# Performance work log

Hardware: AMD Instinct MI355X
Metric: run time of the kernel (lower is better)

Reference implementation:

```python
import jax, jax.numpy as jnp
import numpy as np

B, D, H, T = 8192, 256, 512, 4  # batch, latent dim, hidden units, num IAF transforms


def _made_masks():
    deg_in = np.arange(1, D + 1)                      # input degrees 1..D
    deg_h = 1 + (np.arange(H) % (D - 1))              # hidden degrees in [1, D-1]
    m1 = (deg_h[None, :] >= deg_in[:, None]).astype(np.float32)   # [D, H]
    m2 = (deg_h[None, :] >= deg_h[:, None]).astype(np.float32)    # [H, H]
    mo = (deg_in[None, :] > deg_h[:, None]).astype(np.float32)    # [H, D] strict for outputs
    m3 = np.repeat(mo, 2, axis=1)                     # [H, 2D]: params=2 per dim, interleaved
    return jnp.asarray(m1), jnp.asarray(m2), jnp.asarray(m3)

M1, M2, M3 = _made_masks()


def _made(x, w1, b1, w2, b2, w3, b3):
    h = jax.nn.relu(x @ (w1 * M1) + b1)
    h = jax.nn.relu(h @ (w2 * M2) + b2)
    out = (h @ (w3 * M3) + b3).reshape(x.shape[0], D, 2)
    shift, log_var = out[..., 0], out[..., 1]
    # lstm_flag == False branch of Made.call
    return shift, jnp.tanh(log_var)


def setup_inputs() -> dict:
    key = jax.random.key(0)
    ks = jax.random.split(key, 6)
    s1 = 0.05
    return {
        "mean": jax.random.normal(ks[0], (B, D), jnp.float32),
        "log_var": jax.random.normal(ks[1], (B, D), jnp.float32) * 0.5,
        "eps": jax.random.normal(ks[2], (B, D), jnp.float32),
        "W1": jax.random.normal(ks[3], (T, D, H), jnp.float32) * s1,
        "b1": jnp.zeros((T, H), jnp.float32),
        "W2": jax.random.normal(ks[4], (T, H, H), jnp.float32) * s1,
        "b2": jnp.zeros((T, H), jnp.float32),
        "W3": jax.random.normal(ks[5], (T, H, 2 * D), jnp.float32) * s1,
        "b3": jnp.zeros((T, 2 * D), jnp.float32),
    }


def reference(mean, log_var, eps, W1, b1, W2, b2, W3, b3):
    # Base sample from MultivariateNormalDiag(mean, exp(0.5*log_var))
    x = mean + jnp.exp(0.5 * log_var) * eps
    # Chain([IAF_0, Perm, IAF_1, Perm, ..., IAF_{T-1}, Perm]).forward applies the
    # LAST bijector first: Perm, then Invert(MAF)_{T-1}, ..., down to IAF_0.
    # Invert(MAF).forward == MAF.inverse: a single parallel MADE pass.
    for i in reversed(range(T)):
        x = x[..., ::-1]  # Permute(reversed(range(D)))
        shift, log_scale = _made(x, W1[i], b1[i], W2[i], b2[i], W3[i], b3[i])
        x = (x - shift) * jnp.exp(-log_scale)
    return x
```

## Files before the change

kernel.cpp:

```cpp
#include <hip/hip_runtime.h>


typedef _Float16 f16;
typedef __attribute__((ext_vector_type(8))) _Float16 f16x8;
typedef __attribute__((ext_vector_type(4))) float f32x4;

#define NB 8192
#define ND 256
#define NH 512
#define NT 4
#define XSTR 260

#define W1F_OFF 0
#define W2F_OFF (NT*NH*ND)
#define W3F_OFF (W2F_OFF + NT*NH*NH)
#define WS_ELEMS (W3F_OFF + NT*NH*NH)

__device__ __forceinline__ int h_orig(int j) {
  if (j < 3) return j == 0 ? 0 : (j == 1 ? 255 : 510);
  if (j < 6) return j == 3 ? 1 : (j == 4 ? 256 : 511);
  int d = j >> 1;
  return (j & 1) ? (d + 254) : (d - 1);
}
__device__ __forceinline__ int h_deg(int j) {
  return (j < 3) ? 1 : (j < 6) ? 2 : (j >> 1);
}

__global__ void prep_weights(const float* __restrict__ W1,
                             const float* __restrict__ W2,
                             const float* __restrict__ W3,
                             f16* __restrict__ ws)
{
  int idx = blockIdx.x * blockDim.x + threadIdx.x;
  if (idx >= WS_ELEMS) return;
  float v;
  if (idx < W2F_OFF) {
    int t = idx >> 17, r = idx & ((1 << 17) - 1);
    int e = r & 7, lane = (r >> 3) & 63, ks = (r >> 9) & 7, tile = r >> 12;
    int j = tile * 16 + (lane & 15);
    int k = ks * 32 + (lane >> 4) * 8 + e;
    v = (k <= h_deg(j) - 1) ? W1[t * (ND * NH) + k * NH + h_orig(j)] : 0.f;
  } else if (idx < W3F_OFF) {
    int q = idx - W2F_OFF;
    int t = q >> 18, r = q & ((1 << 18) - 1);
    int e = r & 7, lane = (r >> 3) & 63, ks = (r >> 9) & 15, tile = r >> 13;
    int j = tile * 16 + (lane & 15);
    int k = ks * 32 + (lane >> 4) * 8 + e;
    v = (h_deg(k) <= h_deg(j)) ? W2[t * (NH * NH) + h_orig(k) * NH + h_orig(j)] : 0.f;
  } else {
    int q = idx - W3F_OFF;
    int t = q >> 18, r = q & ((1 << 18) - 1);
    int e = r & 7, lane = (r >> 3) & 63, ks = (r >> 9) & 15, tile = r >> 13;
    int n = tile * 16 + (lane & 15);
    int k = ks * 32 + (lane >> 4) * 8 + e;
    v = (h_deg(k) <= (n >> 1)) ? W3[t * (NH * 2 * ND) + h_orig(k) * (2 * ND) + n] : 0.f;
  }
  ws[idx] = (f16)v;
}

#define MFMA16 __builtin_amdgcn_mfma_f32_16x16x32_f16

template<int SSTRB>
__device__ __forceinline__ void gemm_hybrid(const f16* srcA,
                                            const f16* __restrict__ wtS,
                                            const f16* __restrict__ wtB,
                                            int ncS, int ncB,
                                            int lrow, int lk8,
                                            f32x4 &aS0, f32x4 &aS1,
                                            f32x4 &aB0, f32x4 &aB1)
{
  const f32x4 z = {0.f, 0.f, 0.f, 0.f};
  aS0 = z; aS1 = z; aB0 = z; aB1 = z;
  const int r1 = 16 + lrow;
  const int swz0 = (lrow & 7) << 4;
  const int swz1 = (r1 & 7) << 4;

  f16x8 cS0 = *(const f16x8*)(wtS);
  f16x8 cS1 = *(const f16x8*)(wtS + 512);
  f16x8 cB0 = *(const f16x8*)(wtB);
  f16x8 cB1 = *(const f16x8*)(wtB + 512);
  for (int c = 0; ; ++c) {
    f16x8 nS0, nS1, nB0, nB1;
    const bool more = (c + 1 < ncS);
    if (more) {
      const f16* pS = wtS + (c + 1) * 1024;
      const f16* pB = wtB + (c + 1) * 1024;
      nS0 = *(const f16x8*)(pS);
      nS1 = *(const f16x8*)(pS + 512);
      nB0 = *(const f16x8*)(pB);
      nB1 = *(const f16x8*)(pB + 512);
    }
    #pragma unroll
    for (int u = 0; u < 2; ++u) {
      int kb = 128 * c + u * 64 + lk8 * 16;
      f16x8 a0 = *(const f16x8*)((const char*)srcA + ((lrow * SSTRB + kb) ^ swz0));
      f16x8 a1 = *(const f16x8*)((const char*)srcA + ((r1 * SSTRB + kb) ^ swz1));
      f16x8 bS = u ? cS1 : cS0;
      f16x8 bB = u ? cB1 : cB0;
      aS0 = MFMA16(a0, bS, aS0, 0, 0, 0);
      aS1 = MFMA16(a1, bS, aS1, 0, 0, 0);
      aB0 = MFMA16(a0, bB, aB0, 0, 0, 0);
      aB1 = MFMA16(a1, bB, aB1, 0, 0, 0);
    }
    if (!more) break;
    cS0 = nS0; cS1 = nS1; cB0 = nB0; cB1 = nB1;
  }

  if (ncS < ncB) {
    f16x8 dB0 = *(const f16x8*)(wtB + ncS * 1024);
    f16x8 dB1 = *(const f16x8*)(wtB + ncS * 1024 + 512);
    for (int c = ncS; ; ++c) {
      f16x8 nB0, nB1;
      const bool more = (c + 1 < ncB);
      if (more) {
        const f16* pB = wtB + (c + 1) * 1024;
        nB0 = *(const f16x8*)(pB);
        nB1 = *(const f16x8*)(pB + 512);
      }
      #pragma unroll
      for (int u = 0; u < 2; ++u) {
        int kb = 128 * c + u * 64 + lk8 * 16;
        f16x8 a0 = *(const f16x8*)((const char*)srcA + ((lrow * SSTRB + kb) ^ swz0));
        f16x8 a1 = *(const f16x8*)((const char*)srcA + ((r1 * SSTRB + kb) ^ swz1));
        f16x8 bB = u ? dB1 : dB0;
        aB0 = MFMA16(a0, bB, aB0, 0, 0, 0);
        aB1 = MFMA16(a1, bB, aB1, 0, 0, 0);
      }
      if (!more) break;
      dB0 = nB0; dB1 = nB1;
    }
  }
}

__device__ __forceinline__ void epi_relu_tile(f32x4 a0, f32x4 a1,
                                              const float* __restrict__ bias_t,
                                              f16* dst, int np, int lrow, int lk8)
{
  const bool ev = (lrow & 1) == 0;
  int n = np + lrow;
  float bv = bias_t[h_orig(n)];
  #pragma unroll
  for (int j = 0; j < 4; ++j) {
    float v0 = fmaxf(a0[j] + bv, 0.f);
    float v1 = fmaxf(a1[j] + bv, 0.f);
    float p0 = __shfl_xor(v0, 1);
    float p1 = __shfl_xor(v1, 1);
    float lo = ev ? v0 : p1;
    float hi = ev ? p0 : v1;
    int m = (ev ? 0 : 16) + lk8 * 4 + j;
    int nw = n & ~1;
    unsigned int w = (unsigned int)__builtin_bit_cast(unsigned short, (f16)lo)
                   | ((unsigned int)__builtin_bit_cast(unsigned short, (f16)hi) << 16);
    int off = m * 1024 + nw * 2;
    *(unsigned int*)((char*)dst + (off ^ ((m & 7) << 4))) = w;
  }
}

__global__ __launch_bounds__(1024, 4) void iaf_main(
    const float* __restrict__ mean, const float* __restrict__ logv,
    const float* __restrict__ eps,
    const float* __restrict__ b1, const float* __restrict__ b2,
    const float* __restrict__ b3,
    const f16* __restrict__ ws, float* __restrict__ out)
{
  __shared__ float xbuf[32][XSTR];
  __shared__ __align__(16) f16 buf0[32 * 512];
  __shared__ __align__(16) f16 buf1[32 * 512];

  const int tid = threadIdx.x;
  const int wid = tid >> 6;
  const int lane = tid & 63;
  const int lrow = lane & 15;
  const int lk8 = lane >> 4;
  const int row0 = blockIdx.x * 32;

  const int tS = wid, tB = 31 - wid;
  const int npS = tS * 16, npB = tB * 16;
  const int nc1S = tS / 8 + 1, nc1B = tB / 8 + 1;
  const int nc23S = tS / 4 + 1, nc23B = tB / 4 + 1;

  {
    int m = tid >> 5;
    int c0 = (tid & 31) * 8;
    const int g = (row0 + m) * ND + c0;
    #pragma unroll
    for (int i = 0; i < 8; i += 4) {
      f32x4 mu = *(const f32x4*)(mean + g + i);
      f32x4 lv = *(const f32x4*)(logv + g + i);
      f32x4 ep = *(const f32x4*)(eps + g + i);
      f32x4 x;
      #pragma unroll
      for (int q = 0; q < 4; ++q) x[q] = mu[q] + __expf(0.5f * lv[q]) * ep[q];
      *(f32x4*)(&xbuf[m][c0 + i]) = x;
    }
  }
  __syncthreads();

  for (int t = NT - 1; t >= 0; --t) {
    {
      int m = tid >> 5;
      int k0 = (tid & 31) * 8;
      f32x4 lo = *(const f32x4*)(&xbuf[m][248 - k0]);
      f32x4 hi = *(const f32x4*)(&xbuf[m][252 - k0]);
      f16x8 pk;
      pk[0] = (f16)hi[3]; pk[1] = (f16)hi[2]; pk[2] = (f16)hi[1]; pk[3] = (f16)hi[0];
      pk[4] = (f16)lo[3]; pk[5] = (f16)lo[2]; pk[6] = (f16)lo[1]; pk[7] = (f16)lo[0];
      int off = m * 512 + k0 * 2;
      *(f16x8*)((char*)buf0 + (off ^ ((m & 7) << 4))) = pk;
    }
    __syncthreads();

    f32x4 aS0, aS1, aB0, aB1;

    {
      const f16* w1b = ws + W1F_OFF + t * (NH * ND);
      gemm_hybrid<512>(buf0,
                       w1b + tS * 4096 + lane * 8,
                       w1b + tB * 4096 + lane * 8,
                       nc1S, nc1B, lrow, lk8, aS0, aS1, aB0, aB1);
      epi_relu_tile(aS0, aS1, b1 + t * NH, buf1, npS, lrow, lk8);
      epi_relu_tile(aB0, aB1, b1 + t * NH, buf1, npB, lrow, lk8);
    }
    __syncthreads();

    {
      const f16* w2b = ws + W2F_OFF + t * (NH * NH);
      gemm_hybrid<1024>(buf1,
                        w2b + tS * 8192 + lane * 8,
                        w2b + tB * 8192 + lane * 8,
                        nc23S, nc23B, lrow, lk8, aS0, aS1, aB0, aB1);
      epi_relu_tile(aS0, aS1, b2 + t * NH, buf0, npS, lrow, lk8);
      epi_relu_tile(aB0, aB1, b2 + t * NH, buf0, npB, lrow, lk8);
    }
    __syncthreads();

    {
      const f16* w3b = ws + W3F_OFF + t * (NH * NH);
      gemm_hybrid<1024>(buf0,
                        w3b + tS * 8192 + lane * 8,
                        w3b + tB * 8192 + lane * 8,
                        nc23S, nc23B, lrow, lk8, aS0, aS1, aB0, aB1);

      const bool ev = (lrow & 1) == 0;
      const float* b3t = b3 + t * (2 * ND);
      float xnS[2][4], xnB[2][4];
      #pragma unroll
      for (int pt = 0; pt < 2; ++pt) {
        f32x4 o_0 = pt ? aB0 : aS0;
        f32x4 o_1 = pt ? aB1 : aS1;
        float (*xn)[4] = pt ? xnB : xnS;
        int n = (pt ? npB : npS) + lrow;
        float bv = b3t[n];
        #pragma unroll
        for (int j = 0; j < 4; ++j) {
          float o0 = o_0[j] + bv;
          float o1 = o_1[j] + bv;
          float po0 = __shfl_xor(o0, 1);
          float po1 = __shfl_xor(o1, 1);
          if (ev) {
            int d = n >> 1;
            float xc0 = xbuf[lk8 * 4 + j][255 - d];
            float e0 = __expf(2.f * po0);
            float t0 = 1.f - 2.f / (e0 + 1.f);
            xn[0][j] = (xc0 - o0) * __expf(-t0);
            float xc1 = xbuf[16 + lk8 * 4 + j][255 - d];
            float e1 = __expf(2.f * po1);
            float t1 = 1.f - 2.f / (e1 + 1.f);
            xn[1][j] = (xc1 - o1) * __expf(-t1);
          }
        }
      }
      __syncthreads();
      if (ev) {
        int dS = (npS + lrow) >> 1;
        int dB = (npB + lrow) >> 1;
        #pragma unroll
        for (int j = 0; j < 4; ++j) {
          xbuf[lk8 * 4 + j][dS]      = xnS[0][j];
          xbuf[16 + lk8 * 4 + j][dS] = xnS[1][j];
          xbuf[lk8 * 4 + j][dB]      = xnB[0][j];
          xbuf[16 + lk8 * 4 + j][dB] = xnB[1][j];
        }
      }
      __syncthreads();
    }
  }

  {
    int m = tid >> 5;
    int c0 = (tid & 31) * 8;
    float* op = out + (row0 + m) * ND + c0;
    #pragma unroll
    for (int i = 0; i < 8; i += 4)
      *(f32x4*)(op + i) = *(const f32x4*)(&xbuf[m][c0 + i]);
  }
}

extern "C" void kernel_launch(void* const* d_in, const int* in_sizes, int n_in,
                              void* d_out, int out_size, void* d_ws, size_t ws_size,
                              hipStream_t stream) {
  const float* mean = (const float*)d_in[0];
  const float* logv = (const float*)d_in[1];
  const float* eps  = (const float*)d_in[2];
  const float* W1   = (const float*)d_in[3];
  const float* b1   = (const float*)d_in[4];
  const float* W2   = (const float*)d_in[5];
  const float* b2   = (const float*)d_in[6];
  const float* W3   = (const float*)d_in[7];
  const float* b3   = (const float*)d_in[8];
  f16* ws = (f16*)d_ws;

  prep_weights<<<(WS_ELEMS + 255) / 256, 256, 0, stream>>>(W1, W2, W3, ws);
  iaf_main<<<NB / 32, 1024, 0, stream>>>(mean, logv, eps, b1, b2, b3, ws,
                                         (float*)d_out);
}
```

Baseline: 78.77 us.

## Shrink block to 16 rows with 8 waves each owning four column tiles

Each block now handles 16 batch rows instead of 32 and runs 512 threads instead of 1024. Each of the 8 waves computes two small/big pairs of 16-column tiles with a single 16-row MFMA per tile, so every weight fragment loaded from global feeds half as many MFMAs. The aim is to double the grid size and cut LDS per block, which should improve occupancy and load balance across CUs. The cost is twice the total weight traffic from L2 per output row and less reuse of weights across rows.

```diff
diff --git a/kernel.cpp b/kernel.cpp
--- a/kernel.cpp
+++ b/kernel.cpp
@@ -9,6 +9,7 @@
 #define ND 256
 #define NH 512
 #define NT 4
+#define ROWS 16
 #define XSTR 260
 
 #define W1F_OFF 0
@@ -61,19 +62,16 @@
 #define MFMA16 __builtin_amdgcn_mfma_f32_16x16x32_f16
 
 template<int SSTRB>
-__device__ __forceinline__ void gemm_hybrid(const f16* srcA,
-                                            const f16* __restrict__ wtS,
-                                            const f16* __restrict__ wtB,
-                                            int ncS, int ncB,
-                                            int lrow, int lk8,
-                                            f32x4 &aS0, f32x4 &aS1,
-                                            f32x4 &aB0, f32x4 &aB1)
+__device__ __forceinline__ void gemm_hyb16(const f16* srcA,
+                                           const f16* __restrict__ wtS,
+                                           const f16* __restrict__ wtB,
+                                           int ncS, int ncB,
+                                           int lrow, int lk8,
+                                           f32x4 &aS, f32x4 &aB)
 {
   const f32x4 z = {0.f, 0.f, 0.f, 0.f};
-  aS0 = z; aS1 = z; aB0 = z; aB1 = z;
-  const int r1 = 16 + lrow;
+  aS = z; aB = z;
   const int swz0 = (lrow & 7) << 4;
-  const int swz1 = (r1 & 7) << 4;
 
   f16x8 cS0 = *(const f16x8*)(wtS);
   f16x8 cS1 = *(const f16x8*)(wtS + 512);
@@ -94,13 +92,8 @@
     for (int u = 0; u < 2; ++u) {
       int kb = 128 * c + u * 64 + lk8 * 16;
       f16x8 a0 = *(const f16x8*)((const char*)srcA + ((lrow * SSTRB + kb) ^ swz0));
-      f16x8 a1 = *(const f16x8*)((const char*)srcA + ((r1 * SSTRB + kb) ^ swz1));
-      f16x8 bS = u ? cS1 : cS0;
-      f16x8 bB = u ? cB1 : cB0;
-      aS0 = MFMA16(a0, bS, aS0, 0, 0, 0);
-      aS1 = MFMA16(a1, bS, aS1, 0, 0, 0);
-      aB0 = MFMA16(a0, bB, aB0, 0, 0, 0);
-      aB1 = MFMA16(a1, bB, aB1, 0, 0, 0);
+      aS = MFMA16(a0, u ? cS1 : cS0, aS, 0, 0, 0);
+      aB = MFMA16(a0, u ? cB1 : cB0, aB, 0, 0, 0);
     }
     if (!more) break;
     cS0 = nS0; cS1 = nS1; cB0 = nB0; cB1 = nB1;
@@ -121,10 +114,7 @@
       for (int u = 0; u < 2; ++u) {
         int kb = 128 * c + u * 64 + lk8 * 16;
         f16x8 a0 = *(const f16x8*)((const char*)srcA + ((lrow * SSTRB + kb) ^ swz0));
-        f16x8 a1 = *(const f16x8*)((const char*)srcA + ((r1 * SSTRB + kb) ^ swz1));
-        f16x8 bB = u ? dB1 : dB0;
-        aB0 = MFMA16(a0, bB, aB0, 0, 0, 0);
-        aB1 = MFMA16(a1, bB, aB1, 0, 0, 0);
+        aB = MFMA16(a0, u ? dB1 : dB0, aB, 0, 0, 0);
       }
       if (!more) break;
       dB0 = nB0; dB1 = nB1;
@@ -132,52 +122,52 @@
   }
 }
 
-__device__ __forceinline__ void epi_relu_tile(f32x4 a0, f32x4 a1,
-                                              const float* __restrict__ bias_t,
-                                              f16* dst, int np, int lrow, int lk8)
+__device__ __forceinline__ void epi16(f32x4 a, const float* __restrict__ bias_t,
+                                      f16* dst, int np, int lrow, int lk8)
 {
   const bool ev = (lrow & 1) == 0;
   int n = np + lrow;
   float bv = bias_t[h_orig(n)];
   #pragma unroll
   for (int j = 0; j < 4; ++j) {
-    float v0 = fmaxf(a0[j] + bv, 0.f);
-    float v1 = fmaxf(a1[j] + bv, 0.f);
+    float v0 = fmaxf(a[j] + bv, 0.f);
     float p0 = __shfl_xor(v0, 1);
-    float p1 = __shfl_xor(v1, 1);
-    float lo = ev ? v0 : p1;
-    float hi = ev ? p0 : v1;
-    int m = (ev ? 0 : 16) + lk8 * 4 + j;
-    int nw = n & ~1;
-    unsigned int w = (unsigned int)__builtin_bit_cast(unsigned short, (f16)lo)
-                   | ((unsigned int)__builtin_bit_cast(unsigned short, (f16)hi) << 16);
-    int off = m * 1024 + nw * 2;
-    *(unsigned int*)((char*)dst + (off ^ ((m & 7) << 4))) = w;
-  }
-}
-
-__global__ __launch_bounds__(1024, 4) void iaf_main(
+    if (ev) {
+      int m = lk8 * 4 + j;
+      unsigned int w = (unsigned int)__builtin_bit_cast(unsigned short, (f16)v0)
+                     | ((unsigned int)__builtin_bit_cast(unsigned short, (f16)p0) << 16);
+      int off = m * 1024 + n * 2;
+      *(unsigned int*)((char*)dst + (off ^ ((m & 7) << 4))) = w;
+    }
+  }
+}
+
+__global__ __launch_bounds__(512, 4) void iaf_main(
     const float* __restrict__ mean, const float* __restrict__ logv,
     const float* __restrict__ eps,
     const float* __restrict__ b1, const float* __restrict__ b2,
     const float* __restrict__ b3,
     const f16* __restrict__ ws, float* __restrict__ out)
 {
-  __shared__ float xbuf[32][XSTR];
-  __shared__ __align__(16) f16 buf0[32 * 512];
-  __shared__ __align__(16) f16 buf1[32 * 512];
+  __shared__ float xbuf[ROWS][XSTR];
+  __shared__ __align__(16) f16 buf0[ROWS * 512];
+  __shared__ __align__(16) f16 buf1[ROWS * 512];
 
   const int tid = threadIdx.x;
   const int wid = tid >> 6;
   const int lane = tid & 63;
   const int lrow = lane & 15;
   const int lk8 = lane >> 4;
-  const int row0 = blockIdx.x * 32;
-
-  const int tS = wid, tB = 31 - wid;
-  const int npS = tS * 16, npB = tB * 16;
-  const int nc1S = tS / 8 + 1, nc1B = tB / 8 + 1;
-  const int nc23S = tS / 4 + 1, nc23B = tB / 4 + 1;
+  const int row0 = blockIdx.x * ROWS;
+
+  const int tS1 = 2 * wid,     tB1 = 31 - 2 * wid;
+  const int tS2 = 2 * wid + 1, tB2 = 30 - 2 * wid;
+  const int npS1 = tS1 * 16, npB1 = tB1 * 16;
+  const int npS2 = tS2 * 16, npB2 = tB2 * 16;
+  const int nc1S1 = tS1 / 8 + 1, nc1B1 = tB1 / 8 + 1;
+  const int nc1S2 = tS2 / 8 + 1, nc1B2 = tB2 / 8 + 1;
+  const int nc23S1 = tS1 / 4 + 1, nc23B1 = tB1 / 4 + 1;
+  const int nc23S2 = tS2 / 4 + 1, nc23B2 = tB2 / 4 + 1;
 
   {
     int m = tid >> 5;
@@ -210,76 +200,77 @@
     }
     __syncthreads();
 
-    f32x4 aS0, aS1, aB0, aB1;
+    f32x4 aS1, aB1, aS2, aB2;
 
     {
       const f16* w1b = ws + W1F_OFF + t * (NH * ND);
-      gemm_hybrid<512>(buf0,
-                       w1b + tS * 4096 + lane * 8,
-                       w1b + tB * 4096 + lane * 8,
-                       nc1S, nc1B, lrow, lk8, aS0, aS1, aB0, aB1);
-      epi_relu_tile(aS0, aS1, b1 + t * NH, buf1, npS, lrow, lk8);
-      epi_relu_tile(aB0, aB1, b1 + t * NH, buf1, npB, lrow, lk8);
+      gemm_hyb16<512>(buf0, w1b + tS1 * 4096 + lane * 8,
+                      w1b + tB1 * 4096 + lane * 8, nc1S1, nc1B1, lrow, lk8, aS1, aB1);
+      gemm_hyb16<512>(buf0, w1b + tS2 * 4096 + lane * 8,
+                      w1b + tB2 * 4096 + lane * 8, nc1S2, nc1B2, lrow, lk8, aS2, aB2);
+      const float* bt = b1 + t * NH;
+      epi16(aS1, bt, buf1, npS1, lrow, lk8);
+      epi16(aB1, bt, buf1, npB1, lrow, lk8);
+      epi16(aS2, bt, buf1, npS2, lrow, lk8);
+      epi16(aB2, bt, buf1, npB2, lrow, lk8);
     }
     __syncthreads();
 
     {
       const f16* w2b = ws + W2F_OFF + t * (NH * NH);
-      gemm_hybrid<1024>(buf1,
-                        w2b + tS * 8192 + lane * 8,
-                        w2b + tB * 8192 + lane * 8,
-                        nc23S, nc23B, lrow, lk8, aS0, aS1, aB0, aB1);
-      epi_relu_tile(aS0, aS1, b2 + t * NH, buf0, npS, lrow, lk8);
-      epi_relu_tile(aB0, aB1, b2 + t * NH, buf0, npB, lrow, lk8);
+      gemm_hyb16<1024>(buf1, w2b + tS1 * 8192 + lane * 8,
+                       w2b + tB1 * 8192 + lane * 8, nc23S1, nc23B1, lrow, lk8, aS1, aB1);
+      gemm_hyb16<1024>(buf1, w2b + tS2 * 8192 + lane * 8,
+                       w2b + tB2 * 8192 + lane * 8, nc23S2, nc23B2, lrow, lk8, aS2, aB2);
+      const float* bt = b2 + t * NH;
+      epi16(aS1, bt, buf0, npS1, lrow, lk8);
+      epi16(aB1, bt, buf0, npB1, lrow, lk8);
+      epi16(aS2, bt, buf0, npS2, lrow, lk8);
+      epi16(aB2, bt, buf0, npB2, lrow, lk8);
     }
     __syncthreads();
 
     {
       const f16* w3b = ws + W3F_OFF + t * (NH * NH);
-      gemm_hybrid<1024>(buf0,
-                        w3b + tS * 8192 + lane * 8,
-                        w3b + tB * 8192 + lane * 8,
-                        nc23S, nc23B, lrow, lk8, aS0, aS1, aB0, aB1);
+      gemm_hyb16<1024>(buf0, w3b + tS1 * 8192 + lane * 8,
+                       w3b + tB1 * 8192 + lane * 8, nc23S1, nc23B1, lrow, lk8, aS1, aB1);
+      gemm_hyb16<1024>(buf0, w3b + tS2 * 8192 + lane * 8,
+                       w3b + tB2 * 8192 + lane * 8, nc23S2, nc23B2, lrow, lk8, aS2, aB2);
 
       const bool ev = (lrow & 1) == 0;
       const float* b3t = b3 + t * (2 * ND);
-      float xnS[2][4], xnB[2][4];
+      float xn1S[4], xn1B[4], xn2S[4], xn2B[4];
       #pragma unroll
-      for (int pt = 0; pt < 2; ++pt) {
-        f32x4 o_0 = pt ? aB0 : aS0;
-        f32x4 o_1 = pt ? aB1 : aS1;
-        float (*xn)[4] = pt ? xnB : xnS;
-        int n = (pt ? npB : npS) + lrow;
+      for (int pt = 0; pt < 4; ++pt) {
+        f32x4 ac = (pt == 0) ? aS1 : (pt == 1) ? aB1 : (pt == 2) ? aS2 : aB2;
+        float* xn = (pt == 0) ? xn1S : (pt == 1) ? xn1B : (pt == 2) ? xn2S : xn2B;
+        int np = (pt == 0) ? npS1 : (pt == 1) ? npB1 : (pt == 2) ? npS2 : npB2;
+        int n = np + lrow;
         float bv = b3t[n];
         #pragma unroll
         for (int j = 0; j < 4; ++j) {
-          float o0 = o_0[j] + bv;
-          float o1 = o_1[j] + bv;
-          float po0 = __shfl_xor(o0, 1);
-          float po1 = __shfl_xor(o1, 1);
+          float o = ac[j] + bv;
+          float po = __shfl_xor(o, 1);
           if (ev) {
             int d = n >> 1;
-            float xc0 = xbuf[lk8 * 4 + j][255 - d];
-            float e0 = __expf(2.f * po0);
-            float t0 = 1.f - 2.f / (e0 + 1.f);
-            xn[0][j] = (xc0 - o0) * __expf(-t0);
-            float xc1 = xbuf[16 + lk8 * 4 + j][255 - d];
-            float e1 = __expf(2.f * po1);
-            float t1 = 1.f - 2.f / (e1 + 1.f);
-            xn[1][j] = (xc1 - o1) * __expf(-t1);
+            float xc = xbuf[lk8 * 4 + j][255 - d];
+            float e2 = __expf(2.f * po);
+            float tl = 1.f - 2.f / (e2 + 1.f);
+            xn[j] = (xc - o) * __expf(-tl);
           }
         }
       }
       __syncthreads();
       if (ev) {
-        int dS = (npS + lrow) >> 1;
-        int dB = (npB + lrow) >> 1;
+        int d1S = (npS1 + lrow) >> 1, d1B = (npB1 + lrow) >> 1;
+        int d2S = (npS2 + lrow) >> 1, d2B = (npB2 + lrow) >> 1;
         #pragma unroll
         for (int j = 0; j < 4; ++j) {
-          xbuf[lk8 * 4 + j][dS]      = xnS[0][j];
-          xbuf[16 + lk8 * 4 + j][dS] = xnS[1][j];
-          xbuf[lk8 * 4 + j][dB]      = xnB[0][j];
-          xbuf[16 + lk8 * 4 + j][dB] = xnB[1][j];
+          int m = lk8 * 4 + j;
+          xbuf[m][d1S] = xn1S[j];
+          xbuf[m][d1B] = xn1B[j];
+          xbuf[m][d2S] = xn2S[j];
+          xbuf[m][d2B] = xn2B[j];
         }
       }
       __syncthreads();
@@ -311,6 +302,6 @@
   f16* ws = (f16*)d_ws;
 
   prep_weights<<<(WS_ELEMS + 255) / 256, 256, 0, stream>>>(W1, W2, W3, ws);
-  iaf_main<<<NB / 32, 1024, 0, stream>>>(mean, logv, eps, b1, b2, b3, ws,
-                                         (float*)d_out);
-}
+  iaf_main<<<NB / ROWS, 512, 0, stream>>>(mean, logv, eps, b1, b2, b3, ws,
+                                          (float*)d_out);
+}
```

Result: slower. 160.4 us (+103.7%).
